# Kernel tuning notes

Measured on AMD Instinct MI355X. Metric: run time of the kernel, lower is better.

## Reference

```python
import math
import jax, jax.numpy as jnp
import numpy as np

R, C, B, E = 64, 256, 4, 768
Q, QD = 256, 512
H = 12
D = E // H

def setup_inputs() -> dict:
    key = jax.random.key(0)
    ks = jax.random.split(key, 10)
    def lin(kw, out_d, in_d):
        s = 1.0 / math.sqrt(in_d)
        return jax.random.uniform(kw, (out_d, in_d), jnp.float32, -s, s)
    return {
        "x": jax.random.normal(ks[0], (R, C, B, E), jnp.float32),
        "query": jax.random.normal(ks[1], (Q, B, QD), jnp.float32),
        "Wq": lin(ks[2], E, QD), "bq": jnp.zeros((E,), jnp.float32),
        "Wk": lin(ks[3], E, E), "bk": jnp.zeros((E,), jnp.float32),
        "Wv": lin(ks[4], E, E), "bv": jnp.zeros((E,), jnp.float32),
        "Wo": lin(ks[5], E, E), "bo": jnp.zeros((E,), jnp.float32),
    }

def reference(x, query, Wq, bq, Wk, bk, Wv, bv, Wo, bo):
    # x: (R, C, B, E) rows/cols/batch/embed; query: (Q, B, QD)
    q_cols = query.shape[0]
    scaling = (D ** -0.5) / math.sqrt(q_cols)  # align_scaling over query rows
    q = (query @ Wq.T + bq).reshape(q_cols, B, H, D) * scaling  # (Q,B,H,D)
    k = (x @ Wk.T + bk).reshape(R, C, B, H, D)
    # tied row attention: scores summed over the column axis c
    attn = jnp.einsum("qnhd,rcnhd->hnqr", q, k)  # (H,B,Q,R)
    probs = jax.nn.softmax(attn, axis=-1)
    v = (x @ Wv.T + bv).reshape(R, C, B, H, D)
    # value update: sum attn over query cols q, broadcast over c
    ctx = jnp.einsum("hnqr,rcnhd->rcnhd", probs, v).reshape(R, C, B, E)
    out = ctx @ Wo.T + bo  # (R,C,B,E)
    return out
```

## Files before the change

### kernel.cpp

```cpp
#include <hip/hip_runtime.h>
#include <hip/hip_bf16.h>


typedef __attribute__((ext_vector_type(8))) short bf16x8;
typedef __attribute__((ext_vector_type(4))) float f32x4;

__device__ __forceinline__ void load_lds16(const void* g, void* l) {
    __builtin_amdgcn_global_load_lds(
        (const __attribute__((address_space(1))) void*)g,
        (__attribute__((address_space(3))) void*)l, 16, 0, 0);
}

__global__ __launch_bounds__(256) void prep_kernel(const float* __restrict__ x,
                                                   float* __restrict__ xsp,
                                                   __hip_bfloat16* __restrict__ xb,
                                                   const float* __restrict__ Wv,
                                                   __hip_bfloat16* __restrict__ Wvb,
                                                   const float* __restrict__ Wo,
                                                   __hip_bfloat16* __restrict__ Wob) {
    int b = blockIdx.x, tid = threadIdx.x;
    if (b < 768) {
        int gid = b * 256 + tid;
        int e4 = gid % 192;
        int t2 = gid / 192;
        int rb = t2 & 255;
        int part = t2 >> 8;
        int r = rb >> 2, n = rb & 3;
        size_t base = (size_t)r * 786432 + (size_t)part * 196608 + n * 768 + e4 * 4;
        const float4* px = (const float4*)(x + base);
        ushort* xbu = (ushort*)xb + base;
        float4 s = {0.f, 0.f, 0.f, 0.f};
        #pragma unroll 4
        for (int c = 0; c < 64; ++c) {
            float4 v = px[(size_t)c * 768];
            s.x += v.x; s.y += v.y; s.z += v.z; s.w += v.w;
            union { ushort4 u; __hip_bfloat16 h[4]; } pk;
            pk.h[0] = __float2bfloat16(v.x); pk.h[1] = __float2bfloat16(v.y);
            pk.h[2] = __float2bfloat16(v.z); pk.h[3] = __float2bfloat16(v.w);
            *(ushort4*)(xbu + (size_t)c * 3072) = pk.u;
        }
        *(float4*)(xsp + (size_t)part * 196608 + rb * 768 + e4 * 4) = s;
    } else {
        const float* src = (b < 1344) ? Wv : Wo;
        __hip_bfloat16* dst = (b < 1344) ? Wvb : Wob;
        int i = (b - ((b < 1344) ? 768 : 1344)) * 256 + tid;
        float4 v = ((const float4*)src)[i];
        dst[i * 4 + 0] = __float2bfloat16(v.x);
        dst[i * 4 + 1] = __float2bfloat16(v.y);
        dst[i * 4 + 2] = __float2bfloat16(v.z);
        dst[i * 4 + 3] = __float2bfloat16(v.w);
    }
}

template <int MODE>
__global__ __launch_bounds__(256) void gemm_kernel(const float* __restrict__ A,
                                                   const float* __restrict__ W,
                                                   const float* __restrict__ bias,
                                                   float* __restrict__ Cf,
                                                   int M, int N, int K, int KS, float p0) {
    __shared__ float As[16][65];
    __shared__ float Ws[16][65];
    int tid = threadIdx.x;
    int tx = tid & 15, ty = tid >> 4;
    int m0 = blockIdx.y * 64, n0 = blockIdx.x * 64;
    int z = blockIdx.z;
    int kbeg = z * KS, kend = kbeg + KS;
    float acc[4][4] = {};

    for (int k0 = kbeg; k0 < kend; k0 += 16) {
        #pragma unroll
        for (int i = 0; i < 4; ++i) {
            int idx = tid + 256 * i;
            int mm = idx >> 4, kk = idx & 15;
            size_t ai = (size_t)(m0 + mm) * K + k0 + kk;
            if (MODE == 0)
                As[kk][mm] = A[ai] + A[ai + 196608] + A[ai + 393216] + A[ai + 589824];
            else
                As[kk][mm] = A[ai];
            Ws[kk][mm] = W[(size_t)(n0 + mm) * K + k0 + kk];
        }
        __syncthreads();
        #pragma unroll
        for (int kk = 0; kk < 16; ++kk) {
            float a[4], b[4];
            #pragma unroll
            for (int i = 0; i < 4; ++i) a[i] = As[kk][ty + 16 * i];
            #pragma unroll
            for (int j = 0; j < 4; ++j) b[j] = Ws[kk][tx + 16 * j];
            #pragma unroll
            for (int i = 0; i < 4; ++i)
                #pragma unroll
                for (int j = 0; j < 4; ++j) acc[i][j] += a[i] * b[j];
        }
        __syncthreads();
    }
    float* Cz = Cf + (size_t)z * M * N;
    #pragma unroll
    for (int i = 0; i < 4; ++i) {
        int m = m0 + ty + 16 * i;
        #pragma unroll
        for (int j = 0; j < 4; ++j) {
            int n = n0 + tx + 16 * j;
            float v = acc[i][j];
            if (MODE == 0) Cz[(size_t)m * N + n] = v + ((z == 0) ? p0 * bias[n] : 0.f);
            else           Cz[(size_t)m * N + n] = (v + ((z == 0) ? bias[n] : 0.f)) * p0;
        }
    }
}

__global__ __launch_bounds__(256) void attn_kernel(const float* __restrict__ qp,
                                                   const float* __restrict__ ksum,
                                                   float* __restrict__ psum) {
    int h = blockIdx.x >> 2;
    int n = blockIdx.x & 3;
    __shared__ float kd[64][68];
    __shared__ float qs[4][68];
    __shared__ float sacc[4][64];
    int tid = threadIdx.x;

    #pragma unroll
    for (int it = 0; it < 16; ++it) {
        int idx = tid + 256 * it;
        int r = idx >> 6, d = idx & 63;
        size_t ki = (size_t)(r * 4 + n) * 768 + h * 64 + d;
        kd[r][d] = ksum[ki] + ksum[ki + 196608] + ksum[ki + 393216] + ksum[ki + 589824];
    }
    __syncthreads();

    int wave = tid >> 6, lane = tid & 63;
    float acc = 0.f;
    for (int q = wave; q < 256; q += 4) {
        size_t qi = (size_t)(q * 4 + n) * 768 + h * 64 + lane;
        float qv = qp[qi] + qp[qi + 786432];
        qs[wave][lane] = qv;
        float val = 0.f;
        #pragma unroll
        for (int d4 = 0; d4 < 16; ++d4) {
            float4 kv = *(const float4*)&kd[lane][d4 * 4];
            float4 qq = *(const float4*)&qs[wave][d4 * 4];
            val += qq.x * kv.x + qq.y * kv.y + qq.z * kv.z + qq.w * kv.w;
        }
        float mx = val;
        #pragma unroll
        for (int off = 1; off < 64; off <<= 1) mx = fmaxf(mx, __shfl_xor(mx, off));
        float p = __expf(val - mx);
        float s = p;
        #pragma unroll
        for (int off = 1; off < 64; off <<= 1) s += __shfl_xor(s, off);
        acc += p / s;
    }
    sacc[wave][lane] = acc;
    __syncthreads();
    if (tid < 64) {
        psum[blockIdx.x * 64 + tid] =
            sacc[0][tid] + sacc[1][tid] + sacc[2][tid] + sacc[3][tid];
    }
}


__device__ __forceinline__ int swz(int R, int kg) {
    return ((R >> 1) << 6) + ((((((R & 1) << 2) | kg)) ^ ((R >> 1) & 7)) << 3);
}

template <int MODE>
__global__ __launch_bounds__(512, 2) void mfma_gemm2(const ushort* __restrict__ A,
                                                     const ushort* __restrict__ W,
                                                     const float* __restrict__ bias,
                                                     const float* __restrict__ scale,
                                                     float* __restrict__ Cf,
                                                     __hip_bfloat16* __restrict__ Cb,
                                                     int M, int N, int K) {
    __shared__ short lds[65536];
    const int NT = K >> 5;
    int tid = threadIdx.x;
    int wave = tid >> 6, lane = tid & 63;
    int wr = wave >> 2, wc = wave & 3;
    int r16 = lane & 15, kg = lane >> 4;

    int cpx = gridDim.x >> 3;
    int hh = blockIdx.x;
    int orig = (hh & 7) * cpx + (hh >> 3);
    int nbx = N >> 8;
    int by = orig / nbx, bx = orig - by * nbx;
    int m0 = by << 8, n0 = bx << 8;

    int c0 = tid, c1 = tid + 512;
    int p0c = c0 >> 3, s0c = (c0 & 7) ^ (p0c & 7);
    int row0 = (p0c << 1) | (s0c >> 2), kg0 = s0c & 3;
    int p1c = c1 >> 3, s1c = (c1 & 7) ^ (p1c & 7);
    int row1 = (p1c << 1) | (s1c >> 2), kg1 = s1c & 3;
    const ushort* pA0 = A + (size_t)(m0 + row0) * K + kg0 * 8;
    const ushort* pA1 = A + (size_t)(m0 + row1) * K + kg1 * 8;
    const ushort* pB0 = W + (size_t)(n0 + row0) * K + kg0 * 8;
    const ushort* pB1 = W + (size_t)(n0 + row1) * K + kg1 * 8;
    int dep0 = (wave * 64) * 8;
    int dep1 = (512 + wave * 64) * 8;

    f32x4 acc[8][4];
    #pragma unroll
    for (int i = 0; i < 8; ++i)
        #pragma unroll
        for (int j = 0; j < 4; ++j) acc[i][j] = (f32x4){0.f, 0.f, 0.f, 0.f};

    #pragma unroll
    for (int p = 0; p < 3; ++p) {
        int sb = p * 16384, ko = p * 32;
        load_lds16(pA0 + ko, &lds[sb + dep0]);
        load_lds16(pA1 + ko, &lds[sb + dep1]);
        load_lds16(pB0 + ko, &lds[sb + 8192 + dep0]);
        load_lds16(pB1 + ko, &lds[sb + 8192 + dep1]);
    }

    for (int t = 0; t < NT; ++t) {
        if (t + 2 < NT)      { asm volatile("s_waitcnt vmcnt(8)" ::: "memory"); }
        else if (t + 1 < NT) { asm volatile("s_waitcnt vmcnt(4)" ::: "memory"); }
        else                 { asm volatile("s_waitcnt vmcnt(0)" ::: "memory"); }
        __builtin_amdgcn_s_barrier();
        __builtin_amdgcn_sched_barrier(0);
        const short* sb = &lds[(t & 3) * 16384];
        int s3 = ((t + 3) & 3) * 16384;
        int k3 = (t + 3) * 32;

        bf16x8 bv[4], af[4];
        #pragma unroll
        for (int ni = 0; ni < 4; ++ni)
            bv[ni] = *(const bf16x8*)&sb[8192 + swz(wc * 64 + ni * 16 + r16, kg)];
        #pragma unroll
        for (int mi = 0; mi < 4; ++mi)
            af[mi] = *(const bf16x8*)&sb[swz(wr * 128 + mi * 16 + r16, kg)];
        if (t + 3 < NT) {
            load_lds16(pA0 + k3, &lds[s3 + dep0]);
            load_lds16(pA1 + k3, &lds[s3 + dep1]);
        }
        __builtin_amdgcn_s_setprio(1);
        #pragma unroll
        for (int mi = 0; mi < 4; ++mi)
            #pragma unroll
            for (int ni = 0; ni < 4; ++ni)
                acc[mi][ni] = __builtin_amdgcn_mfma_f32_16x16x32_bf16(
                    af[mi], bv[ni], acc[mi][ni], 0, 0, 0);
        __builtin_amdgcn_s_setprio(0);

        #pragma unroll
        for (int mi = 0; mi < 4; ++mi)
            af[mi] = *(const bf16x8*)&sb[swz(wr * 128 + 64 + mi * 16 + r16, kg)];
        if (t + 3 < NT) {
            load_lds16(pB0 + k3, &lds[s3 + 8192 + dep0]);
            load_lds16(pB1 + k3, &lds[s3 + 8192 + dep1]);
        }
        __builtin_amdgcn_s_setprio(1);
        #pragma unroll
        for (int mi = 0; mi < 4; ++mi)
            #pragma unroll
            for (int ni = 0; ni < 4; ++ni)
                acc[4 + mi][ni] = __builtin_amdgcn_mfma_f32_16x16x32_bf16(
                    af[mi], bv[ni], acc[4 + mi][ni], 0, 0, 0);
        __builtin_amdgcn_s_setprio(0);
    }

    int col = lane & 15, rbase = (lane >> 4) << 2;
    #pragma unroll
    for (int ni = 0; ni < 4; ++ni) {
        int gn = n0 + wc * 64 + ni * 16 + col;
        float bn = bias[gn];
        #pragma unroll
        for (int mi = 0; mi < 8; ++mi) {
            int gmb = m0 + wr * 128 + mi * 16 + rbase;
            #pragma unroll
            for (int i = 0; i < 4; ++i) {
                int gm = gmb + i;
                float v = acc[mi][ni][i] + bn;
                if (MODE == 2) {
                    float sc = scale[(((gn >> 6) << 2) + (gm & 3)) * 64 + (gm >> 10)];
                    Cb[(size_t)gm * N + gn] = __float2bfloat16(v * sc);
                } else {
                    Cf[(size_t)gm * N + gn] = v;
                }
            }
        }
    }
}

extern "C" void kernel_launch(void* const* d_in, const int* in_sizes, int n_in,
                              void* d_out, int out_size, void* d_ws, size_t ws_size,
                              hipStream_t stream) {
    const float* x     = (const float*)d_in[0];
    const float* query = (const float*)d_in[1];
    const float* Wq    = (const float*)d_in[2];
    const float* bq    = (const float*)d_in[3];
    const float* Wk    = (const float*)d_in[4];
    const float* bk    = (const float*)d_in[5];
    const float* Wv    = (const float*)d_in[6];
    const float* bv    = (const float*)d_in[7];
    const float* Wo    = (const float*)d_in[8];
    const float* bo    = (const float*)d_in[9];
    float* out = (float*)d_out;

    __hip_bfloat16* xb   = (__hip_bfloat16*)d_ws;
    __hip_bfloat16* vtmp = xb + 50331648;
    __hip_bfloat16* Wvb  = vtmp + 50331648;
    __hip_bfloat16* Wob  = Wvb + 589824;
    float* ksum = (float*)(Wob + 589824);
    float* qp   = ksum + 786432;
    float* psum = qp + 1572864;
    float* xsp = (float*)vtmp;

    prep_kernel<<<1920, 256, 0, stream>>>(x, xsp, xb, Wv, Wvb, Wo, Wob);
    gemm_kernel<0><<<dim3(12, 4, 4), 256, 0, stream>>>(xsp, Wk, bk, ksum, 256, 768, 768, 192, 256.0f);
    gemm_kernel<1><<<dim3(12, 16, 2), 256, 0, stream>>>(query, Wq, bq, qp, 1024, 768, 512, 256, 0.0078125f);
    attn_kernel<<<48, 256, 0, stream>>>(qp, ksum, psum);
    mfma_gemm2<2><<<768, 512, 0, stream>>>(
        (const ushort*)xb, (const ushort*)Wvb, bv, psum, nullptr, vtmp, 65536, 768, 768);
    mfma_gemm2<3><<<768, 512, 0, stream>>>(
        (const ushort*)vtmp, (const ushort*)Wob, bo, nullptr, out, nullptr, 65536, 768, 768);
}
```

Measured before the change: 677.8 us.

## Split attention over query chunks, widen Q-GEMM split-K, stage GEMM epilogue via LDS

The attention kernel now splits the query loop into four chunks, so it launches 192 blocks instead of 48. It writes partial probability sums that the MODE 2 epilogue adds together. The Q projection GEMM uses a 4-way K split, and attention sums four partials. The main MFMA GEMM issues both A and B prefetches before its LDS fragment reads. Its epilogue stages results through swizzled LDS so global stores are coalesced 16-byte vectors. These changes target low occupancy in the small kernels and scattered scalar stores in the big GEMMs, at the cost of extra barriers and extra partial-sum reads.

```diff
diff --git a/kernel.cpp b/kernel.cpp
--- a/kernel.cpp
+++ b/kernel.cpp
@@ -111,8 +111,10 @@
 __global__ __launch_bounds__(256) void attn_kernel(const float* __restrict__ qp,
                                                    const float* __restrict__ ksum,
                                                    float* __restrict__ psum) {
-    int h = blockIdx.x >> 2;
-    int n = blockIdx.x & 3;
+    int qpart = blockIdx.x / 48;
+    int hn = blockIdx.x % 48;
+    int h = hn >> 2;
+    int n = hn & 3;
     __shared__ float kd[64][68];
     __shared__ float qs[4][68];
     __shared__ float sacc[4][64];
@@ -129,9 +131,9 @@
 
     int wave = tid >> 6, lane = tid & 63;
     float acc = 0.f;
-    for (int q = wave; q < 256; q += 4) {
+    for (int q = qpart * 64 + wave; q < qpart * 64 + 64; q += 4) {
         size_t qi = (size_t)(q * 4 + n) * 768 + h * 64 + lane;
-        float qv = qp[qi] + qp[qi + 786432];
+        float qv = qp[qi] + qp[qi + 786432] + qp[qi + 1572864] + qp[qi + 2359296];
         qs[wave][lane] = qv;
         float val = 0.f;
         #pragma unroll
@@ -221,17 +223,20 @@
         int s3 = ((t + 3) & 3) * 16384;
         int k3 = (t + 3) * 32;
 
-        bf16x8 bv[4], af[4];
-        #pragma unroll
-        for (int ni = 0; ni < 4; ++ni)
-            bv[ni] = *(const bf16x8*)&sb[8192 + swz(wc * 64 + ni * 16 + r16, kg)];
-        #pragma unroll
-        for (int mi = 0; mi < 4; ++mi)
-            af[mi] = *(const bf16x8*)&sb[swz(wr * 128 + mi * 16 + r16, kg)];
         if (t + 3 < NT) {
             load_lds16(pA0 + k3, &lds[s3 + dep0]);
             load_lds16(pA1 + k3, &lds[s3 + dep1]);
-        }
+            load_lds16(pB0 + k3, &lds[s3 + 8192 + dep0]);
+            load_lds16(pB1 + k3, &lds[s3 + 8192 + dep1]);
+        }
+
+        bf16x8 bv[4], af[4];
+        #pragma unroll
+        for (int ni = 0; ni < 4; ++ni)
+            bv[ni] = *(const bf16x8*)&sb[8192 + swz(wc * 64 + ni * 16 + r16, kg)];
+        #pragma unroll
+        for (int mi = 0; mi < 4; ++mi)
+            af[mi] = *(const bf16x8*)&sb[swz(wr * 128 + mi * 16 + r16, kg)];
         __builtin_amdgcn_s_setprio(1);
         #pragma unroll
         for (int mi = 0; mi < 4; ++mi)
@@ -244,10 +249,6 @@
         #pragma unroll
         for (int mi = 0; mi < 4; ++mi)
             af[mi] = *(const bf16x8*)&sb[swz(wr * 128 + 64 + mi * 16 + r16, kg)];
-        if (t + 3 < NT) {
-            load_lds16(pB0 + k3, &lds[s3 + 8192 + dep0]);
-            load_lds16(pB1 + k3, &lds[s3 + 8192 + dep1]);
-        }
         __builtin_amdgcn_s_setprio(1);
         #pragma unroll
         for (int mi = 0; mi < 4; ++mi)
@@ -258,24 +259,68 @@
         __builtin_amdgcn_s_setprio(0);
     }
 
-    int col = lane & 15, rbase = (lane >> 4) << 2;
-    #pragma unroll
-    for (int ni = 0; ni < 4; ++ni) {
-        int gn = n0 + wc * 64 + ni * 16 + col;
-        float bn = bias[gn];
-        #pragma unroll
-        for (int mi = 0; mi < 8; ++mi) {
-            int gmb = m0 + wr * 128 + mi * 16 + rbase;
-            #pragma unroll
-            for (int i = 0; i < 4; ++i) {
-                int gm = gmb + i;
-                float v = acc[mi][ni][i] + bn;
-                if (MODE == 2) {
-                    float sc = scale[(((gn >> 6) << 2) + (gm & 3)) * 64 + (gm >> 10)];
-                    Cb[(size_t)gm * N + gn] = __float2bfloat16(v * sc);
-                } else {
-                    Cf[(size_t)gm * N + gn] = v;
+    int col = lane & 15, rq = lane >> 4;
+
+    if (MODE == 2) {
+        __syncthreads();
+        __hip_bfloat16* eb = (__hip_bfloat16*)lds;
+        #pragma unroll
+        for (int ni = 0; ni < 4; ++ni) {
+            int lgn = wc * 64 + ni * 16 + col;
+            int gn = n0 + lgn;
+            float bn = bias[gn];
+            #pragma unroll
+            for (int mi = 0; mi < 8; ++mi) {
+                #pragma unroll
+                for (int i = 0; i < 4; ++i) {
+                    int lr = wr * 128 + mi * 16 + rq * 4 + i;
+                    int gm = m0 + lr;
+                    int si = (((gn >> 6) << 2) + (gm & 3)) * 64 + (gm >> 10);
+                    float sc = scale[si] + scale[si + 3072] +
+                               scale[si + 6144] + scale[si + 9216];
+                    float v = (acc[mi][ni][i] + bn) * sc;
+                    eb[lr * 256 + (lgn ^ (((lr >> 2) & 3) << 4))] = __float2bfloat16(v);
                 }
+            }
+        }
+        __syncthreads();
+        #pragma unroll
+        for (int it = 0; it < 16; ++it) {
+            int c = it * 512 + tid;
+            int row = c >> 5, cc = c & 31;
+            int pc = cc ^ (((row >> 2) & 3) << 1);
+            bf16x8 vv = *(const bf16x8*)&lds[row * 256 + pc * 8];
+            *(bf16x8*)(void*)&Cb[(size_t)(m0 + row) * N + n0 + cc * 8] = vv;
+        }
+    } else {
+        float* ef = (float*)lds;
+        #pragma unroll
+        for (int p = 0; p < 2; ++p) {
+            __syncthreads();
+            if (wr == p) {
+                #pragma unroll
+                for (int ni = 0; ni < 4; ++ni) {
+                    int lgn = wc * 64 + ni * 16 + col;
+                    float bn = bias[n0 + lgn];
+                    #pragma unroll
+                    for (int mi = 0; mi < 8; ++mi) {
+                        #pragma unroll
+                        for (int i = 0; i < 4; ++i) {
+                            int lr = mi * 16 + rq * 4 + i;
+                            float v = acc[mi][ni][i] + bn;
+                            ef[lr * 256 + (lgn ^ (((lr >> 2) & 3) << 4))] = v;
+                        }
+                    }
+                }
+            }
+            __syncthreads();
+            #pragma unroll
+            for (int it = 0; it < 16; ++it) {
+                int c = it * 512 + tid;
+                int row = c >> 6, cc = c & 63;
+                int pc = cc ^ (((row >> 2) & 3) << 2);
+                float4 vv = *(const float4*)&ef[row * 256 + pc * 4];
+                *(float4*)&Cf[(size_t)(m0 + p * 128 + row) * N + n0 + cc * 4] = vv;
             }
         }
     }
@@ -302,13 +347,13 @@
     __hip_bfloat16* Wob  = Wvb + 589824;
     float* ksum = (float*)(Wob + 589824);
     float* qp   = ksum + 786432;
-    float* psum = qp + 1572864;
+    float* psum = qp + 3145728;
     float* xsp = (float*)vtmp;
 
     prep_kernel<<<1920, 256, 0, stream>>>(x, xsp, xb, Wv, Wvb, Wo, Wob);
     gemm_kernel<0><<<dim3(12, 4, 4), 256, 0, stream>>>(xsp, Wk, bk, ksum, 256, 768, 768, 192, 256.0f);
-    gemm_kernel<1><<<dim3(12, 16, 2), 256, 0, stream>>>(query, Wq, bq, qp, 1024, 768, 512, 256, 0.0078125f);
-    attn_kernel<<<48, 256, 0, stream>>>(qp, ksum, psum);
+    gemm_kernel<1><<<dim3(12, 16, 4), 256, 0, stream>>>(query, Wq, bq, qp, 1024, 768, 512, 128, 0.0078125f);
+    attn_kernel<<<192, 256, 0, stream>>>(qp, ksum, psum);
     mfma_gemm2<2><<<768, 512, 0, stream>>>(
         (const ushort*)xb, (const ushort*)Wvb, bv, psum, nullptr, vtmp, 65536, 768, 768);
     mfma_gemm2<3><<<768, 512, 0, stream>>>(
```

Result: faster. 608.8 us (-10.2%).
